# Kernel optimization log

Hardware: AMD Instinct MI355X
Metric: run time of the kernel (lower is better)

Reference implementation:

```python
import jax, jax.numpy as jnp
import numpy as np

DIM = 768
HEADS = 12


def setup_inputs() -> dict:
    key = jax.random.key(0)
    ks = jax.random.split(key, 8)
    B, N, M, C, H = 8, 1024, 1024, DIM, HEADS
    x = jax.random.normal(ks[0], (B, N, C), dtype=jnp.float32)
    context = jax.random.normal(ks[1], (B, M, C), dtype=jnp.float32)
    s = 1.0 / np.sqrt(C)
    Wq = jax.random.normal(ks[2], (C, C), dtype=jnp.float32) * s
    Wkv = jax.random.normal(ks[3], (C, 2 * C), dtype=jnp.float32) * s
    # depthwise 3x3 conv over attention map: OIHW with I=1 (groups=H)
    conv_w = jax.random.normal(ks[4], (H, 1, 3, 3), dtype=jnp.float32) * (1.0 / 3.0)
    conv_b = jax.random.normal(ks[5], (H,), dtype=jnp.float32) * 0.02
    Wp = jax.random.normal(ks[6], (C, C), dtype=jnp.float32) * s
    bp = jax.random.normal(ks[7], (C,), dtype=jnp.float32) * 0.02
    return {"x": x, "context": context, "Wq": Wq, "Wkv": Wkv,
            "conv_w": conv_w, "conv_b": conv_b, "Wp": Wp, "bp": bp}


def reference(x, context, Wq, Wkv, conv_w, conv_b, Wp, bp):
    B, N, C = x.shape
    H = conv_w.shape[0]
    d = C // H
    scale = d ** (-0.5)
    # projections
    q = (x @ Wq).reshape(B, N, H, d).transpose(0, 2, 1, 3)          # [B,H,N,d]
    kv = (context @ Wkv).reshape(B, -1, 2, H, d)
    k = kv[:, :, 0].transpose(0, 2, 1, 3)                            # [B,H,M,d]
    v = kv[:, :, 1].transpose(0, 2, 1, 3)                            # [B,H,M,d]
    # attention scores + softmax over keys
    attn = jnp.einsum('bhnd,bhmd->bhnm', q, k) * scale               # [B,H,N,M]
    attn = jax.nn.softmax(attn, axis=-1)
    # depthwise 3x3 conv on the attention map (heads = channels)
    attn = jax.lax.conv_general_dilated(
        attn, conv_w, window_strides=(1, 1), padding='SAME',
        feature_group_count=H,
        dimension_numbers=('NCHW', 'OIHW', 'NCHW'))
    attn = attn + conv_b[None, :, None, None]
    # attend values, merge heads, output projection
    out = jnp.einsum('bhnm,bhmd->bhnd', attn, v)                     # [B,H,N,d]
    out = out.transpose(0, 2, 1, 3).reshape(B, N, C)
    return out @ Wp + bp
```

## Files before the change

kernel.cpp:

```cpp
#include <hip/hip_runtime.h>
#include <hip/hip_bf16.h>

typedef __hip_bfloat16 bf16;
typedef __hip_bfloat162 bf162;

#define B_ 8
#define N_ 1024
#define M_ 1024
#define C_ 768
#define H_ 12
#define D_ 64
#define YST 1032

typedef __attribute__((ext_vector_type(8))) short short8v;
typedef __attribute__((ext_vector_type(4))) float f32x4;

__device__ __forceinline__ float bf2f(bf16 v){ return __bfloat162float(v); }
__device__ __forceinline__ bf16 f2bf(float v){ return __float2bfloat16(v); }

__device__ __forceinline__ void gl_lds16(const bf16* g, bf16* l){
  __builtin_amdgcn_global_load_lds((const __attribute__((address_space(1))) unsigned*)g,
                                   (__attribute__((address_space(3))) unsigned*)l, 16, 0, 0);
}

__global__ __launch_bounds__(256)
void prep_all(const float* __restrict__ x, const float* __restrict__ ctx,
              bf16* __restrict__ xb, bf16* __restrict__ ctxb,
              const float* __restrict__ Wq, const float* __restrict__ Wkv,
              const float* __restrict__ Wp,
              bf16* __restrict__ Wqt, bf16* __restrict__ Wkvt, bf16* __restrict__ Wpt)
{
  __shared__ float tile[32][33];
  int bid = blockIdx.x;
  if (bid < 6144){
    int i = bid*256 + threadIdx.x;
    const float* src; bf16* dst; int j;
    if (i < 786432){ src = x;   dst = xb;   j = i; }
    else           { src = ctx; dst = ctxb; j = i - 786432; }
    const float4* ip = reinterpret_cast<const float4*>(src) + 2*(size_t)j;
    float4 a = ip[0], b = ip[1];
    union { uint4 u; bf16 h[8]; } pk;
    pk.h[0]=f2bf(a.x); pk.h[1]=f2bf(a.y); pk.h[2]=f2bf(a.z); pk.h[3]=f2bf(a.w);
    pk.h[4]=f2bf(b.x); pk.h[5]=f2bf(b.y); pk.h[6]=f2bf(b.z); pk.h[7]=f2bf(b.w);
    reinterpret_cast<uint4*>(dst)[j] = pk.u;
    return;
  }
  bid -= 6144;
  const float* W; bf16* Wt; int N, bx, by;
  if (bid < 576)       { W = Wq;  Wt = Wqt;  N = 768;  bx = bid % 24;  by = bid / 24; }
  else if (bid < 1728) { int r = bid - 576;  W = Wkv; Wt = Wkvt; N = 1536; bx = r % 48; by = r / 48; }
  else                 { int r = bid - 1728; W = Wp;  Wt = Wpt;  N = 768;  bx = r % 24; by = r / 24; }
  const int K = 768;
  const int n0 = bx*32, k0 = by*32;
  const int tx = threadIdx.x & 31, ty = threadIdx.x >> 5;
#pragma unroll
  for (int i=0;i<32;i+=8) tile[ty+i][tx] = W[(size_t)(k0+ty+i)*N + n0+tx];
  __syncthreads();
#pragma unroll
  for (int i=0;i<32;i+=8) Wt[(size_t)(n0+ty+i)*K + k0+tx] = f2bf(tile[tx][ty+i]);
}

__global__ __launch_bounds__(1024)
void yprep(bf16* __restrict__ Vt, bf16* __restrict__ Y0, bf16* __restrict__ Y1,
           float* __restrict__ SV, const float* __restrict__ conv_w)
{
  __shared__ bf16 sm[64*YST];
  const int t = threadIdx.x;
  const int bh = blockIdx.x;
  const int h = bh % H_;
  const size_t pbase = (size_t)bh * 65536;

  float w[9];
#pragma unroll
  for (int q=0;q<9;q++) w[q] = conv_w[h*9+q];

#pragma unroll
  for (int k=0;k<8;k++){
    int idx = k*8192 + t*8;
    int d = idx >> 10, m = idx & 1023;
    *reinterpret_cast<uint4*>(&sm[d*YST + m]) = *reinterpret_cast<const uint4*>(Vt + pbase + idx);
  }
  __syncthreads();

  {
    const int d = t >> 4, j = t & 15;
    float s = 0.f;
#pragma unroll
    for (int k=0;k<8;k++){
      union { uint4 u; bf16 hh[8]; } mv;
      mv.u = *reinterpret_cast<const uint4*>(&sm[d*YST + j*64 + k*8]);
#pragma unroll
      for (int e=0;e<8;e++) s += bf2f(mv.hh[e]);
    }
    s += __shfl_xor(s, 1); s += __shfl_xor(s, 2);
    s += __shfl_xor(s, 4); s += __shfl_xor(s, 8);
    if (j == 0) SV[bh*64 + d] = s;
  }

  const int d    = (t & 255) >> 2;
  const int blkS = t & 3;
  const int xb   = (d >> 1) & 3;
  const int mbb  = t >> 8;
#pragma unroll
  for (int k=0;k<8;k++){
    const int c  = k*1024 + t;
    const int mb = k*4 + mbb;
    const int m0 = mb*32 + ((blkS ^ xb) << 3);
    const int base = d*YST + m0;
    union { uint4 u; bf16 hh[8]; } mv;
    mv.u = *reinterpret_cast<const uint4*>(&sm[base]);
    float v[8];
#pragma unroll
    for (int e=0;e<8;e++) v[e] = bf2f(mv.hh[e]);
    float vl = (m0 == 0)    ? 0.f : bf2f(sm[base-1]);
    float vr = (m0 == 1016) ? 0.f : bf2f(sm[base+8]);

    union { uint4 u; bf16 hh[8]; } o0, o1, o2;
#pragma unroll
    for (int m=0;m<8;m++){
      float vm1 = (m==0) ? vl : v[m-1];
      float vp1 = (m==7) ? vr : v[m+1];
      o0.hh[m] = f2bf(w[0]*vp1 + w[1]*v[m] + w[2]*vm1);
      o1.hh[m] = f2bf(w[3]*vp1 + w[4]*v[m] + w[5]*vm1);
      o2.hh[m] = f2bf(w[6]*vp1 + w[7]*v[m] + w[8]*vm1);
    }
    const size_t go = pbase + (size_t)c*8;
    *reinterpret_cast<uint4*>(Y0 + go) = o0.u;
    *reinterpret_cast<uint4*>(Y1 + go) = o1.u;
    *reinterpret_cast<uint4*>(Vt + go) = o2.u;
  }
}

__global__ __launch_bounds__(256)
void gemm_qkv(const bf16* __restrict__ A0, const bf16* __restrict__ A1,
              const bf16* __restrict__ Bt0, const bf16* __restrict__ Bt1,
              bf16* __restrict__ outQ, bf16* __restrict__ outK, bf16* __restrict__ outV)
{
  __shared__ bf16 As[128*32];
  __shared__ bf16 Bs[128*32];
  const int K = 768;

  const int nwg = 1152, cpx = nwg >> 3;
  int bid = blockIdx.x;
  bid = (bid & 7)*cpx + (bid >> 3);
  const int rowb = bid / 18, colb = bid - rowb*18;
  const int row0 = rowb*128;
  const bool isQ = (colb < 6);
  const int c0 = isQ ? colb*128 : (colb-6)*128;

  const int t = threadIdx.x;
  const int w = t>>6, l = t&63, lr = l&15, g = l>>4;
  const int wr = w>>1, wc = w&1;

  const bf16* Ap = (isQ ? A0 : A1) + (size_t)row0*K;
  const bf16* Bp = (isQ ? Bt0 : Bt1) + (size_t)c0*K;
  const int srow = t>>2;
  const int schunk = (t&3)*8;

  f32x4 acc[4][4];
#pragma unroll
  for (int mi=0;mi<4;mi++)
#pragma unroll
    for (int ni=0;ni<4;ni++) acc[mi][ni] = (f32x4){0.f,0.f,0.f,0.f};

  for (int k0 = 0; k0 < K; k0 += 32){
    gl_lds16(Ap + (size_t)srow*K      + k0 + schunk, As + t*8);
    gl_lds16(Ap + (size_t)(srow+64)*K + k0 + schunk, As + 2048 + t*8);
    gl_lds16(Bp + (size_t)srow*K      + k0 + schunk, Bs + t*8);
    gl_lds16(Bp + (size_t)(srow+64)*K + k0 + schunk, Bs + 2048 + t*8);
    __syncthreads();

    short8v a[4], b[4];
#pragma unroll
    for (int mi=0;mi<4;mi++)
      a[mi] = *reinterpret_cast<const short8v*>(&As[(wr*64+mi*16+lr)*32 + g*8]);
#pragma unroll
    for (int ni=0;ni<4;ni++)
      b[ni] = *reinterpret_cast<const short8v*>(&Bs[(wc*64+ni*16+lr)*32 + g*8]);
#pragma unroll
    for (int mi=0;mi<4;mi++)
#pragma unroll
      for (int ni=0;ni<4;ni++)
        acc[mi][ni] = __builtin_amdgcn_mfma_f32_16x16x32_bf16(a[mi], b[ni], acc[mi][ni], 0,0,0);
    __syncthreads();
  }

  if (isQ){
#pragma unroll
    for (int mi=0;mi<4;mi++)
#pragma unroll
      for (int ni=0;ni<4;ni++){
        int c = c0 + wc*64 + ni*16 + lr;
        int h = c >> 6, dd = c & 63;
#pragma unroll
        for (int q=0;q<4;q++){
          int grow = row0 + wr*64 + mi*16 + g*4 + q;
          int b = grow >> 10, n = grow & 1023;
          outQ[((((size_t)b*H_ + h)*N_ + n)<<6) + dd] = f2bf(acc[mi][ni][q] * 0.18033688f);
        }
      }
  } else {
#pragma unroll
    for (int mi=0;mi<4;mi++)
#pragma unroll
      for (int ni=0;ni<4;ni++){
        int c = c0 + wc*64 + ni*16 + lr;
        if (c < 768){
          int h = c >> 6, dd = c & 63;
#pragma unroll
          for (int q=0;q<4;q++){
            int grow = row0 + wr*64 + mi*16 + g*4 + q;
            int b = grow >> 10, m = grow & 1023;
            int eidx = ((m>>4)<<10) + ((dd>>3)<<7) + ((m&15)<<3) + (dd&7);
            outK[((size_t)b*H_ + h)*65536 + eidx] = f2bf(acc[mi][ni][q]);
          }
        } else {
          int cc = c - 768;
          int h = cc >> 6, dd = cc & 63;
          int grow = row0 + wr*64 + mi*16 + g*4;
          int b = grow >> 10, m = grow & 1023;
          union { ushort4 u; bf16 hh[4]; } pk;
#pragma unroll
          for (int q=0;q<4;q++) pk.hh[q] = f2bf(acc[mi][ni][q]);
          size_t off = (((size_t)b*H_ + h)*D_ + dd)*(size_t)M_ + m;
          *reinterpret_cast<ushort4*>(&outV[off]) = pk.u;
        }
      }
  }
}

__global__ __launch_bounds__(256)
void gemm_out(const bf16* __restrict__ A, const bf16* __restrict__ Bt,
              const float* __restrict__ bias, float* __restrict__ outf)
{
  __shared__ bf16 As[128*32];
  __shared__ bf16 Bs[128*32];
  const int K = 768;

  const int nwg = 384, cpx = nwg >> 3;
  int bid = blockIdx.x;
  bid = (bid & 7)*cpx + (bid >> 3);
  const int rowb = bid / 6, colb = bid - rowb*6;
  const int row0 = rowb*128, c0 = colb*128;

  const int t = threadIdx.x;
  const int w = t>>6, l = t&63, lr = l&15, g = l>>4;
  const int wr = w>>1, wc = w&1;

  const bf16* Ap = A + (size_t)row0*K;
  const bf16* Bp = Bt + (size_t)c0*K;
  const int srow = t>>2;
  const int schunk = (t&3)*8;

  f32x4 acc[4][4];
#pragma unroll
  for (int mi=0;mi<4;mi++)
#pragma unroll
    for (int ni=0;ni<4;ni++) acc[mi][ni] = (f32x4){0.f,0.f,0.f,0.f};

  for (int k0 = 0; k0 < K; k0 += 32){
    gl_lds16(Ap + (size_t)srow*K      + k0 + schunk, As + t*8);
    gl_lds16(Ap + (size_t)(srow+64)*K + k0 + schunk, As + 2048 + t*8);
    gl_lds16(Bp + (size_t)srow*K      + k0 + schunk, Bs + t*8);
    gl_lds16(Bp + (size_t)(srow+64)*K + k0 + schunk, Bs + 2048 + t*8);
    __syncthreads();

    short8v a[4], b[4];
#pragma unroll
    for (int mi=0;mi<4;mi++)
      a[mi] = *reinterpret_cast<const short8v*>(&As[(wr*64+mi*16+lr)*32 + g*8]);
#pragma unroll
    for (int ni=0;ni<4;ni++)
      b[ni] = *reinterpret_cast<const short8v*>(&Bs[(wc*64+ni*16+lr)*32 + g*8]);
#pragma unroll
    for (int mi=0;mi<4;mi++)
#pragma unroll
      for (int ni=0;ni<4;ni++)
        acc[mi][ni] = __builtin_amdgcn_mfma_f32_16x16x32_bf16(a[mi], b[ni], acc[mi][ni], 0,0,0);
    __syncthreads();
  }

  float bv[4];
#pragma unroll
  for (int ni=0;ni<4;ni++) bv[ni] = bias[c0 + wc*64 + ni*16 + lr];
#pragma unroll
  for (int mi=0;mi<4;mi++)
#pragma unroll
    for (int ni=0;ni<4;ni++){
      int c = c0 + wc*64 + ni*16 + lr;
#pragma unroll
      for (int q=0;q<4;q++){
        int grow = row0 + wr*64 + mi*16 + g*4 + q;
        outf[(size_t)grow*C_ + c] = acc[mi][ni][q] + bv[ni];
      }
    }
}

__global__ __launch_bounds__(512, 2)
void attn_coop(const bf16* __restrict__ Qb, const bf16* __restrict__ Kb,
               const bf16* __restrict__ Y0, const bf16* __restrict__ Y1,
               const bf16* __restrict__ Y2, const float* __restrict__ SV,
               const float* __restrict__ conv_b, bf16* __restrict__ midb,
               float* __restrict__ E0, float* __restrict__ E127,
               float* __restrict__ X0, float* __restrict__ X1)
{
  __shared__ char smem[49152];
  bf16* sK  = reinterpret_cast<bf16*>(smem);
  bf16* sY  = reinterpret_cast<bf16*>(smem + 8192);
  bf16* Psh = reinterpret_cast<bf16*>(smem + 32768);
  bf16*  smOut = reinterpret_cast<bf16*>(smem);
  float* linvs = reinterpret_cast<float*>(smem + 32768);
  float* eU0   = linvs + 128;
  float* eU2   = eU0 + 256;

  const int t = threadIdx.x, w = t>>6, l = t&63, lr = l&15, g = l>>4;
  const int qp = w & 3, dtp = w >> 2;
  int bid2 = (blockIdx.x & 7)*96 + (blockIdx.x >> 3);
  const int bh = bid2 >> 3, tile = bid2 & 7;
  const int b = bh / H_, h = bh - b*H_;
  const int n0 = tile*128;

  const bf16* Qp  = Qb + (size_t)bh*65536;
  const bf16* Kp  = Kb + (size_t)bh*65536;
  const bf16* Y0p = Y0 + (size_t)bh*65536;
  const bf16* Y1p = Y1 + (size_t)bh*65536;
  const bf16* Y2p = Y2 + (size_t)bh*65536;
  const float cbv = conv_b[h];

  const bf16* qpp = Qp + (size_t)(n0 + w*16 + lr)*D_ + g*8;
  short8v qf0 = *reinterpret_cast<const short8v*>(qpp);
  short8v qf1 = *reinterpret_cast<const short8v*>(qpp + 32);

  float lsum = 0.f;
  f32x4 U[2][3][2];
#pragma unroll
  for (int s2=0;s2<2;s2++)
#pragma unroll
    for (int y=0;y<3;y++)
#pragma unroll
      for (int dl=0;dl<2;dl++) U[s2][y][dl] = (f32x4){0.f,0.f,0.f,0.f};

  const int pkey = lr & 7;
  const int yswz = (lr >> 1) & 3;

  gl_lds16(Kp  + t*8, sK + t*8);
  gl_lds16(Y0p + t*8, sY + t*8);
  gl_lds16(Y1p + t*8, sY + 4096 + t*8);
  gl_lds16(Y2p + t*8, sY + 8192 + t*8);
  asm volatile("s_waitcnt vmcnt(0)" ::: "memory");
  __builtin_amdgcn_s_barrier();

  for (int mc = 0; mc < 16; ++mc){
    f32x4 s[4];
    __builtin_amdgcn_s_setprio(1);
#pragma unroll
    for (int st=0; st<4; ++st){
      const int ka = st*1024 + g*128 + lr*8;
      short8v k0 = *reinterpret_cast<const short8v*>(&sK[ka]);
      short8v k1 = *reinterpret_cast<const short8v*>(&sK[ka + 512]);
      f32x4 a = (f32x4){0.f,0.f,0.f,0.f};
      a = __builtin_amdgcn_mfma_f32_16x16x32_bf16(k0, qf0, a, 0,0,0);
      a = __builtin_amdgcn_mfma_f32_16x16x32_bf16(k1, qf1, a, 0,0,0);
      s[st] = a;
    }
    __builtin_amdgcn_s_setprio(0);

    float psum = 0.f;
#pragma unroll
    for (int st=0; st<4; ++st){
      union { ushort4 u; bf16 hh[4]; } pk;
#pragma unroll
      for (int q=0;q<4;q++){
        float p = exp2f(s[st][q]);
        psum += p;
        pk.hh[q] = f2bf(p);
      }
      const int gran = (st*2 + (g>>1)) ^ pkey;
      *reinterpret_cast<ushort4*>(&Psh[(w*16+lr)*64 + gran*8 + (g&1)*4]) = pk.u;
    }
    lsum += psum;

    asm volatile("s_waitcnt vmcnt(0) lgkmcnt(0)" ::: "memory");
    __builtin_amdgcn_s_barrier();

    if (mc < 15) gl_lds16(Kp + (size_t)(mc+1)*4096 + t*8, sK + t*8);

    __builtin_amdgcn_s_setprio(1);
#pragma unroll
    for (int ks=0; ks<2; ++ks){
      const int agr = ((ks*4 + g) ^ pkey) << 3;
      short8v a0 = *reinterpret_cast<const short8v*>(&Psh[(qp*32      + lr)*64 + agr]);
      short8v a1 = *reinterpret_cast<const short8v*>(&Psh[(qp*32 + 16 + lr)*64 + agr]);
#pragma unroll
      for (int dl=0; dl<2; ++dl){
        const int dd = dtp*32 + dl*16 + lr;
        const int ya = ks*2048 + (dd<<5) + ((g ^ yswz)<<3);
        short8v b0 = *reinterpret_cast<const short8v*>(&sY[ya]);
        short8v b1 = *reinterpret_cast<const short8v*>(&sY[4096 + ya]);
        short8v b2 = *reinterpret_cast<const short8v*>(&sY[8192 + ya]);
        U[0][0][dl] = __builtin_amdgcn_mfma_f32_16x16x32_bf16(a0, b0, U[0][0][dl], 0,0,0);
        U[1][0][dl] = __builtin_amdgcn_mfma_f32_16x16x32_bf16(a1, b0, U[1][0][dl], 0,0,0);
        U[0][1][dl] = __builtin_amdgcn_mfma_f32_16x16x32_bf16(a0, b1, U[0][1][dl], 0,0,0);
        U[1][1][dl] = __builtin_amdgcn_mfma_f32_16x16x32_bf16(a1, b1, U[1][1][dl], 0,0,0);
        U[0][2][dl] = __builtin_amdgcn_mfma_f32_16x16x32_bf16(a0, b2, U[0][2][dl], 0,0,0);
        U[1][2][dl] = __builtin_amdgcn_mfma_f32_16x16x32_bf16(a1, b2, U[1][2][dl], 0,0,0);
      }
    }
    __builtin_amdgcn_s_setprio(0);

    asm volatile("s_waitcnt vmcnt(0)" ::: "memory");
    __builtin_amdgcn_s_barrier();

    if (mc < 15){
      const size_t off = (size_t)(mc+1)*4096 + t*8;
      gl_lds16(Y0p + off, sY + t*8);
      gl_lds16(Y1p + off, sY + 4096 + t*8);
      gl_lds16(Y2p + off, sY + 8192 + t*8);
    }
  }

  lsum += __shfl_xor(lsum, 16);
  lsum += __shfl_xor(lsum, 32);
  if (g == 0) linvs[w*16 + lr] = 1.f / lsum;
  __syncthreads();

#pragma unroll
  for (int s2=0;s2<2;s2++){
    const f32x4 lv = *reinterpret_cast<const f32x4*>(&linvs[qp*32 + s2*16 + g*4]);
#pragma unroll
    for (int y=0;y<3;y++)
#pragma unroll
      for (int dl=0;dl<2;dl++)
#pragma unroll
        for (int q=0;q<4;q++) U[s2][y][dl][q] *= lv[q];
  }

  float sv[2];
#pragma unroll
  for (int dl=0;dl<2;dl++) sv[dl] = SV[bh*64 + dtp*32 + dl*16 + lr];

  if (g == 3){
#pragma unroll
    for (int dl=0;dl<2;dl++) eU0[qp*64 + dtp*32 + dl*16 + lr] = U[1][0][dl][3];
  }
  if (g == 0){
#pragma unroll
    for (int dl=0;dl<2;dl++) eU2[qp*64 + dtp*32 + dl*16 + lr] = U[0][2][dl][0];
  }
  __syncthreads();

#pragma unroll
  for (int dl=0; dl<2; ++dl){
    const int d = dtp*32 + dl*16 + lr;
    const float base = cbv*sv[dl];

    float d0s0 = __shfl(U[0][0][dl][3], (l - 16) & 63);
    float d0s1 = __shfl(U[1][0][dl][3], (l - 16) & 63);
    float u2w0 = __shfl(U[0][2][dl][0], (l + 16) & 63);
    float u2w1 = __shfl(U[1][2][dl][0], (l + 16) & 63);

    {
      float u0s = g ? d0s0 : (qp > 0 ? eU0[(qp-1)*64 + d] : 0.f);
      float u2s = (g < 3) ? u2w0 : u2w1;
      float o0 = u0s            + U[0][1][dl][0] + U[0][2][dl][1] + base;
      float o1 = U[0][0][dl][0] + U[0][1][dl][1] + U[0][2][dl][2] + base;
      float o2 = U[0][0][dl][1] + U[0][1][dl][2] + U[0][2][dl][3] + base;
      float o3 = U[0][0][dl][2] + U[0][1][dl][3] + u2s            + base;
      const int r0 = qp*32 + g*4;
      smOut[(r0+0)*64 + d] = f2bf(o0);
      smOut[(r0+1)*64 + d] = f2bf(o1);
      smOut[(r0+2)*64 + d] = f2bf(o2);
      smOut[(r0+3)*64 + d] = f2bf(o3);
    }
    {
      float u0s = g ? d0s1 : d0s0;
      float u2s = (g < 3) ? u2w1 : (qp < 3 ? eU2[(qp+1)*64 + d] : 0.f);
      float o0 = u0s            + U[1][1][dl][0] + U[1][2][dl][1] + base;
      float o1 = U[1][0][dl][0] + U[1][1][dl][1] + U[1][2][dl][2] + base;
      float o2 = U[1][0][dl][1] + U[1][1][dl][2] + U[1][2][dl][3] + base;
      float o3 = U[1][0][dl][2] + U[1][1][dl][3] + u2s            + base;
      const int r0 = qp*32 + 16 + g*4;
      smOut[(r0+0)*64 + d] = f2bf(o0);
      smOut[(r0+1)*64 + d] = f2bf(o1);
      smOut[(r0+2)*64 + d] = f2bf(o2);
      smOut[(r0+3)*64 + d] = f2bf(o3);
    }

    const int ei = (bh*8 + tile)*64 + d;
    if (qp == 0 && g == 0){
      E0[ei] = U[0][1][dl][0] + U[0][2][dl][1] + base;
      X1[ei] = U[0][2][dl][0];
    }
    if (qp == 3 && g == 3){
      E127[ei] = U[1][0][dl][2] + U[1][1][dl][3] + base;
      X0[ei]   = U[1][0][dl][3];
    }
  }
  __syncthreads();

  {
    const int row = t >> 2, seg = t & 3;
    const bf16* src = smOut + row*64 + seg*16;
    uint4 v0 = *reinterpret_cast<const uint4*>(src);
    uint4 v1 = *reinterpret_cast<const uint4*>(src + 8);
    bf16* dst = midb + ((size_t)b*N_ + n0 + row)*C_ + h*D_ + seg*16;
    *reinterpret_cast<uint4*>(dst)     = v0;
    *reinterpret_cast<uint4*>(dst + 8) = v1;
  }
}

__global__ __launch_bounds__(256)
void edge_patch(const float* __restrict__ E0, const float* __restrict__ E127,
                const float* __restrict__ X0, const float* __restrict__ X1,
                bf16* __restrict__ midb)
{
  int idx = blockIdx.x*256 + threadIdx.x;
  int d = idx & 63;
  int rs = (idx >> 6) & 1;
  int tile = (idx >> 7) & 7;
  int bh = idx >> 10;
  int b = bh / H_, h = bh - b*H_;
  int n0 = tile*128;
  float v; int n;
  if (rs == 0){
    v = E0[(bh*8+tile)*64 + d] + (tile > 0 ? X0[(bh*8+tile-1)*64 + d] : 0.f);
    n = n0;
  } else {
    v = E127[(bh*8+tile)*64 + d] + (tile < 7 ? X1[(bh*8+tile+1)*64 + d] : 0.f);
    n = n0 + 127;
  }
  midb[((size_t)b*N_ + n)*C_ + h*D_ + d] = f2bf(v);
}

extern "C" void kernel_launch(void* const* d_in, const int* in_sizes, int n_in,
                              void* d_out, int out_size, void* d_ws, size_t ws_size,
                              hipStream_t stream) {
  const float* x     = (const float*)d_in[0];
  const float* ctx   = (const float*)d_in[1];
  const float* Wq    = (const float*)d_in[2];
  const float* Wkv   = (const float*)d_in[3];
  const float* convw = (const float*)d_in[4];
  const float* convb = (const float*)d_in[5];
  const float* Wp    = (const float*)d_in[6];
  const float* bp    = (const float*)d_in[7];
  float* out = (float*)d_out;

  char* ws = (char*)d_ws;
  bf16* buf0 = (bf16*)(ws);
  bf16* Wqt  = (bf16*)(ws + 12582912);
  bf16* Wkvt = (bf16*)(ws + 13762560);
  bf16* Wpt  = (bf16*)(ws + 16121856);
  bf16* Qb   = (bf16*)(ws + 17301504);
  bf16* Kb   = (bf16*)(ws + 29884416);
  bf16* Vt   = (bf16*)(ws + 42467328);
  float* SVb = (float*)(ws + 55050240);
  float* E0  = (float*)(ws + 55074816);
  float* E127= (float*)(ws + 55271424);
  float* X0  = (float*)(ws + 55468032);
  float* X1  = (float*)(ws + 55664640);

  bf16* xb = (bf16*)d_out;
  bf16* Y0 = (bf16*)d_out;
  bf16* Y1 = (bf16*)((char*)d_out + 12582912);

  prep_all<<<8448, 256, 0, stream>>>(x, ctx, xb, buf0, Wq, Wkv, Wp, Wqt, Wkvt, Wpt);

  gemm_qkv<<<1152, 256, 0, stream>>>(xb, buf0, Wqt, Wkvt, Qb, Kb, Vt);

  yprep<<<96, 1024, 0, stream>>>(Vt, Y0, Y1, SVb, convw);

  attn_coop<<<768, 512, 0, stream>>>(Qb, Kb, Y0, Y1, Vt, SVb, convb, buf0,
                                     E0, E127, X0, X1);
  edge_patch<<<384, 256, 0, stream>>>(E0, E127, X0, X1, buf0);

  gemm_out<<<384, 256, 0, stream>>>(buf0, Wpt, bp, out);
}
```

Measured before the change: 155.9 us.

## Widen GEMM K-step to 64 and split QK^T across key halves for fragment reuse

Both projection GEMMs now stage two 32-wide K slices per iteration, which halves the number of barrier pairs per tile and doubles shared memory per block. In the attention kernel each wave now computes a 32-query by 32-key score block instead of 16 queries by 64 keys, so every loaded K fragment feeds two MFMAs against two query fragments. Because each wave now covers only half the keys, row sums are kept per query fragment and combined across the two key halves through shared memory, which adds one barrier. The aim is fewer LDS reads and synchronisations per MFMA, at the cost of more registers and extra LDS traffic in the epilogue.

```diff
diff --git a/kernel.cpp b/kernel.cpp
--- a/kernel.cpp
+++ b/kernel.cpp
@@ -136,8 +136,8 @@
               const bf16* __restrict__ Bt0, const bf16* __restrict__ Bt1,
               bf16* __restrict__ outQ, bf16* __restrict__ outK, bf16* __restrict__ outV)
 {
-  __shared__ bf16 As[128*32];
-  __shared__ bf16 Bs[128*32];
+  __shared__ bf16 As[2*4096];
+  __shared__ bf16 Bs[2*4096];
   const int K = 768;
 
   const int nwg = 1152, cpx = nwg >> 3;
@@ -163,25 +163,31 @@
 #pragma unroll
     for (int ni=0;ni<4;ni++) acc[mi][ni] = (f32x4){0.f,0.f,0.f,0.f};
 
-  for (int k0 = 0; k0 < K; k0 += 32){
-    gl_lds16(Ap + (size_t)srow*K      + k0 + schunk, As + t*8);
-    gl_lds16(Ap + (size_t)(srow+64)*K + k0 + schunk, As + 2048 + t*8);
-    gl_lds16(Bp + (size_t)srow*K      + k0 + schunk, Bs + t*8);
-    gl_lds16(Bp + (size_t)(srow+64)*K + k0 + schunk, Bs + 2048 + t*8);
+  for (int k0 = 0; k0 < K; k0 += 64){
+#pragma unroll
+    for (int ks=0; ks<2; ++ks){
+      gl_lds16(Ap + (size_t)srow*K      + k0 + ks*32 + schunk, As + ks*4096 + t*8);
+      gl_lds16(Ap + (size_t)(srow+64)*K + k0 + ks*32 + schunk, As + ks*4096 + 2048 + t*8);
+      gl_lds16(Bp + (size_t)srow*K      + k0 + ks*32 + schunk, Bs + ks*4096 + t*8);
+      gl_lds16(Bp + (size_t)(srow+64)*K + k0 + ks*32 + schunk, Bs + ks*4096 + 2048 + t*8);
+    }
     __syncthreads();
 
-    short8v a[4], b[4];
-#pragma unroll
-    for (int mi=0;mi<4;mi++)
-      a[mi] = *reinterpret_cast<const short8v*>(&As[(wr*64+mi*16+lr)*32 + g*8]);
-#pragma unroll
-    for (int ni=0;ni<4;ni++)
-      b[ni] = *reinterpret_cast<const short8v*>(&Bs[(wc*64+ni*16+lr)*32 + g*8]);
-#pragma unroll
-    for (int mi=0;mi<4;mi++)
+#pragma unroll
+    for (int ks=0; ks<2; ++ks){
+      short8v a[4], b[4];
+#pragma unroll
+      for (int mi=0;mi<4;mi++)
+        a[mi] = *reinterpret_cast<const short8v*>(&As[ks*4096 + (wr*64+mi*16+lr)*32 + g*8]);
 #pragma unroll
       for (int ni=0;ni<4;ni++)
-        acc[mi][ni] = __builtin_amdgcn_mfma_f32_16x16x32_bf16(a[mi], b[ni], acc[mi][ni], 0,0,0);
+        b[ni] = *reinterpret_cast<const short8v*>(&Bs[ks*4096 + (wc*64+ni*16+lr)*32 + g*8]);
+#pragma unroll
+      for (int mi=0;mi<4;mi++)
+#pragma unroll
+        for (int ni=0;ni<4;ni++)
+          acc[mi][ni] = __builtin_amdgcn_mfma_f32_16x16x32_bf16(a[mi], b[ni], acc[mi][ni], 0,0,0);
+    }
     __syncthreads();
   }
 
@@ -233,8 +239,8 @@
 void gemm_out(const bf16* __restrict__ A, const bf16* __restrict__ Bt,
               const float* __restrict__ bias, float* __restrict__ outf)
 {
-  __shared__ bf16 As[128*32];
-  __shared__ bf16 Bs[128*32];
+  __shared__ bf16 As[2*4096];
+  __shared__ bf16 Bs[2*4096];
   const int K = 768;
 
   const int nwg = 384, cpx = nwg >> 3;
@@ -258,25 +264,31 @@
 #pragma unroll
     for (int ni=0;ni<4;ni++) acc[mi][ni] = (f32x4){0.f,0.f,0.f,0.f};
 
-  for (int k0 = 0; k0 < K; k0 += 32){
-    gl_lds16(Ap + (size_t)srow*K      + k0 + schunk, As + t*8);
-    gl_lds16(Ap + (size_t)(srow+64)*K + k0 + schunk, As + 2048 + t*8);
-    gl_lds16(Bp + (size_t)srow*K      + k0 + schunk, Bs + t*8);
-    gl_lds16(Bp + (size_t)(srow+64)*K + k0 + schunk, Bs + 2048 + t*8);
+  for (int k0 = 0; k0 < K; k0 += 64){
+#pragma unroll
+    for (int ks=0; ks<2; ++ks){
+      gl_lds16(Ap + (size_t)srow*K      + k0 + ks*32 + schunk, As + ks*4096 + t*8);
+      gl_lds16(Ap + (size_t)(srow+64)*K + k0 + ks*32 + schunk, As + ks*4096 + 2048 + t*8);
+      gl_lds16(Bp + (size_t)srow*K      + k0 + ks*32 + schunk, Bs + ks*4096 + t*8);
+      gl_lds16(Bp + (size_t)(srow+64)*K + k0 + ks*32 + schunk, Bs + ks*4096 + 2048 + t*8);
+    }
     __syncthreads();
 
-    short8v a[4], b[4];
-#pragma unroll
-    for (int mi=0;mi<4;mi++)
-      a[mi] = *reinterpret_cast<const short8v*>(&As[(wr*64+mi*16+lr)*32 + g*8]);
-#pragma unroll
-    for (int ni=0;ni<4;ni++)
-      b[ni] = *reinterpret_cast<const short8v*>(&Bs[(wc*64+ni*16+lr)*32 + g*8]);
-#pragma unroll
-    for (int mi=0;mi<4;mi++)
+#pragma unroll
+    for (int ks=0; ks<2; ++ks){
+      short8v a[4], b[4];
+#pragma unroll
+      for (int mi=0;mi<4;mi++)
+        a[mi] = *reinterpret_cast<const short8v*>(&As[ks*4096 + (wr*64+mi*16+lr)*32 + g*8]);
 #pragma unroll
       for (int ni=0;ni<4;ni++)
-        acc[mi][ni] = __builtin_amdgcn_mfma_f32_16x16x32_bf16(a[mi], b[ni], acc[mi][ni], 0,0,0);
+        b[ni] = *reinterpret_cast<const short8v*>(&Bs[ks*4096 + (wc*64+ni*16+lr)*32 + g*8]);
+#pragma unroll
+      for (int mi=0;mi<4;mi++)
+#pragma unroll
+        for (int ni=0;ni<4;ni++)
+          acc[mi][ni] = __builtin_amdgcn_mfma_f32_16x16x32_bf16(a[mi], b[ni], acc[mi][ni], 0,0,0);
+    }
     __syncthreads();
   }
 
@@ -308,13 +320,15 @@
   bf16* sK  = reinterpret_cast<bf16*>(smem);
   bf16* sY  = reinterpret_cast<bf16*>(smem + 8192);
   bf16* Psh = reinterpret_cast<bf16*>(smem + 32768);
-  bf16*  smOut = reinterpret_cast<bf16*>(smem);
-  float* linvs = reinterpret_cast<float*>(smem + 32768);
-  float* eU0   = linvs + 128;
-  float* eU2   = eU0 + 256;
+  bf16*  smOut   = reinterpret_cast<bf16*>(smem);
+  float* linvs   = reinterpret_cast<float*>(smem + 32768);
+  float* partial = linvs + 128;
+  float* eU0     = partial + 256;
+  float* eU2     = eU0 + 256;
 
   const int t = threadIdx.x, w = t>>6, l = t&63, lr = l&15, g = l>>4;
   const int qp = w & 3, dtp = w >> 2;
+  const int kf = w >> 2, qg = w & 3;
   int bid2 = (blockIdx.x & 7)*96 + (blockIdx.x >> 3);
   const int bh = bid2 >> 3, tile = bid2 & 7;
   const int b = bh / H_, h = bh - b*H_;
@@ -327,11 +341,15 @@
   const bf16* Y2p = Y2 + (size_t)bh*65536;
   const float cbv = conv_b[h];
 
-  const bf16* qpp = Qp + (size_t)(n0 + w*16 + lr)*D_ + g*8;
-  short8v qf0 = *reinterpret_cast<const short8v*>(qpp);
-  short8v qf1 = *reinterpret_cast<const short8v*>(qpp + 32);
-
-  float lsum = 0.f;
+  short8v qfr[2][2];
+#pragma unroll
+  for (int qf2=0; qf2<2; ++qf2){
+    const bf16* qpp = Qp + (size_t)(n0 + qg*32 + qf2*16 + lr)*D_ + g*8;
+    qfr[qf2][0] = *reinterpret_cast<const short8v*>(qpp);
+    qfr[qf2][1] = *reinterpret_cast<const short8v*>(qpp + 32);
+  }
+
+  float lsq[2] = {0.f, 0.f};
   f32x4 U[2][3][2];
 #pragma unroll
   for (int s2=0;s2<2;s2++)
@@ -351,34 +369,39 @@
   __builtin_amdgcn_s_barrier();
 
   for (int mc = 0; mc < 16; ++mc){
-    f32x4 s[4];
+    f32x4 s[2][2];
     __builtin_amdgcn_s_setprio(1);
 #pragma unroll
-    for (int st=0; st<4; ++st){
-      const int ka = st*1024 + g*128 + lr*8;
-      short8v k0 = *reinterpret_cast<const short8v*>(&sK[ka]);
-      short8v k1 = *reinterpret_cast<const short8v*>(&sK[ka + 512]);
-      f32x4 a = (f32x4){0.f,0.f,0.f,0.f};
-      a = __builtin_amdgcn_mfma_f32_16x16x32_bf16(k0, qf0, a, 0,0,0);
-      a = __builtin_amdgcn_mfma_f32_16x16x32_bf16(k1, qf1, a, 0,0,0);
-      s[st] = a;
+    for (int kfr=0; kfr<2; ++kfr){
+      const int ka = (kf*2 + kfr)*1024 + g*128 + lr*8;
+      short8v k0v = *reinterpret_cast<const short8v*>(&sK[ka]);
+      short8v k1v = *reinterpret_cast<const short8v*>(&sK[ka + 512]);
+#pragma unroll
+      for (int qf2=0; qf2<2; ++qf2){
+        f32x4 a = (f32x4){0.f,0.f,0.f,0.f};
+        a = __builtin_amdgcn_mfma_f32_16x16x32_bf16(k0v, qfr[qf2][0], a, 0,0,0);
+        a = __builtin_amdgcn_mfma_f32_16x16x32_bf16(k1v, qfr[qf2][1], a, 0,0,0);
+        s[kfr][qf2] = a;
+      }
     }
     __builtin_amdgcn_s_setprio(0);
 
-    float psum = 0.f;
-#pragma unroll
-    for (int st=0; st<4; ++st){
-      union { ushort4 u; bf16 hh[4]; } pk;
-#pragma unroll
-      for (int q=0;q<4;q++){
-        float p = exp2f(s[st][q]);
-        psum += p;
-        pk.hh[q] = f2bf(p);
+#pragma unroll
+    for (int kfr=0; kfr<2; ++kfr)
+#pragma unroll
+      for (int qf2=0; qf2<2; ++qf2){
+        union { ushort4 u; bf16 hh[4]; } pk;
+        float ps = 0.f;
+#pragma unroll
+        for (int ri=0;ri<4;ri++){
+          float p = exp2f(s[kfr][qf2][ri]);
+          ps += p;
+          pk.hh[ri] = f2bf(p);
+        }
+        lsq[qf2] += ps;
+        const int gran = (kf*4 + kfr*2 + (g>>1)) ^ pkey;
+        *reinterpret_cast<ushort4*>(&Psh[(qg*32 + qf2*16 + lr)*64 + gran*8 + (g&1)*4]) = pk.u;
       }
-      const int gran = (st*2 + (g>>1)) ^ pkey;
-      *reinterpret_cast<ushort4*>(&Psh[(w*16+lr)*64 + gran*8 + (g&1)*4]) = pk.u;
-    }
-    lsum += psum;
 
     asm volatile("s_waitcnt vmcnt(0) lgkmcnt(0)" ::: "memory");
     __builtin_amdgcn_s_barrier();
@@ -419,9 +442,17 @@
     }
   }
 
-  lsum += __shfl_xor(lsum, 16);
-  lsum += __shfl_xor(lsum, 32);
-  if (g == 0) linvs[w*16 + lr] = 1.f / lsum;
+#pragma unroll
+  for (int qf2=0; qf2<2; ++qf2){
+    lsq[qf2] += __shfl_xor(lsq[qf2], 16);
+    lsq[qf2] += __shfl_xor(lsq[qf2], 32);
+  }
+  if (g == 0){
+    partial[kf*128 + qg*32 + 0*16 + lr] = lsq[0];
+    partial[kf*128 + qg*32 + 1*16 + lr] = lsq[1];
+  }
+  __syncthreads();
+  if (t < 128) linvs[t] = 1.f / (partial[t] + partial[128 + t]);
   __syncthreads();
 
 #pragma unroll
```

Result: slower. 169.7 us (+8.8%).
